# Performance work log

Hardware: AMD Instinct MI355X
Metric: run time of the kernel (lower is better)

Reference implementation:

```python
import jax, jax.numpy as jnp
import numpy as np

GAMMA = 0.9  # decay (init kwarg)


def setup_inputs() -> dict:
    key = jax.random.key(0)
    k0, k1, k2, k3 = jax.random.split(key, 4)
    B, T, D = 16, 2048, 256
    x = jax.random.normal(k0, (B, T, D), jnp.float32)
    scale = 1.0 / np.sqrt(D)
    Wq = jax.random.normal(k1, (D, D), jnp.float32) * scale
    Wk = jax.random.normal(k2, (D, D), jnp.float32) * scale
    Wv = jax.random.normal(k3, (D, D), jnp.float32) * scale
    return {"x": x, "Wq": Wq, "Wk": Wk, "Wv": Wv}


def reference(x, Wq, Wk, Wv):
    # x: [B, T, D]
    B, T, D = x.shape
    Q = x @ Wq  # [B, T, D]
    K = x @ Wk
    V = x @ Wv

    # Sequential retention recurrence over the [D, D] state:
    #   s[t] = gamma * s[t-1] + K[:, t, :]^T @ V[:, t, :]   (sums over batch, as in source)
    Kt = jnp.swapaxes(K, 0, 1)  # [T, B, D]
    Vt = jnp.swapaxes(V, 0, 1)  # [T, B, D]

    def step(s, kv):
        k_t, v_t = kv  # each [B, D]
        s = GAMMA * s + k_t.T @ v_t  # [D, D]
        return s, s.sum(-1)  # emit row-sum [D]

    # Loop runs t = 1 .. T-1 in the source (s starts at 0); s[0] := s[1].
    init = jnp.zeros((D, D), x.dtype)
    _, rows = jax.lax.scan(step, init, (Kt[1:], Vt[1:]))  # rows: [T-1, D]
    S = jnp.concatenate([rows[:1], rows], axis=0)  # [T, D]

    # Faithful to tf.reshape(S, [-1, seq_len]) then tf.transpose: a reshape-scramble,
    # NOT a plain transpose of S.
    S2 = S.reshape(D, T).T  # [T, D]
    return S2[None, :, :] * Q  # broadcast over batch -> [B, T, D]
```

## Files before the change

### kernel.cpp

```cpp
#include <hip/hip_runtime.h>
#include <hip/hip_bf16.h>
#include <math.h>


#define GAMMA_F 0.9f
#define T_LEN 2048
#define D_DIM 256
#define B_DIM 16
#define NCHUNK 32
#define CHUNK 64

typedef __attribute__((ext_vector_type(8))) short bf16x8;
typedef __attribute__((ext_vector_type(16))) float f32x16;

__device__ inline ushort f2bf(float f) {
    union { float f; unsigned u; } v; v.f = f;
    unsigned r = (v.u + 0x7FFFu + ((v.u >> 16) & 1u)) >> 16;
    return (ushort)r;
}

__global__ __launch_bounds__(256) void k_prep(const float* __restrict__ Wq,
                                              const float* __restrict__ Wk,
                                              const float* __restrict__ Wv,
                                              ushort* __restrict__ WqT,
                                              ushort* __restrict__ WkT,
                                              float* __restrict__ wv_sum) {
    int bid = blockIdx.x;
    int tid = threadIdx.x;
    if (bid < 32) {
        __shared__ float tile[64][68];
        const float* W = (bid < 16) ? Wq : Wk;
        ushort* WT = (bid < 16) ? WqT : WkT;
        int b = bid & 15;
        int k0 = (b & 3) * 64;
        int n0 = (b >> 2) * 64;
        int r = tid >> 4;
        int c4 = (tid & 15) * 4;
#pragma unroll
        for (int i = 0; i < 4; ++i) {
            float4 v = *(const float4*)(W + (size_t)(k0 + r + 16 * i) * D_DIM + n0 + c4);
            *(float4*)&tile[r + 16 * i][c4] = v;
        }
        __syncthreads();
        int n = tid >> 2;
        int j0 = (tid & 3) * 16;
        ushort tmp[16];
#pragma unroll
        for (int i = 0; i < 16; ++i) tmp[i] = f2bf(tile[j0 + i][n]);
        ushort* dst = WT + (size_t)(n0 + n) * D_DIM + k0 + j0;
#pragma unroll
        for (int i = 0; i < 16; ++i) dst[i] = tmp[i];
    } else {
        int j = (bid - 32) * 64 + (tid >> 2);
        int q = tid & 3;
        const float4* row4 = (const float4*)(Wv + (size_t)j * D_DIM + q * 64);
        float s = 0.f;
#pragma unroll
        for (int i = 0; i < 16; ++i) {
            float4 v = row4[i];
            s += v.x + v.y + v.z + v.w;
        }
        s += __shfl_xor(s, 1, 64);
        s += __shfl_xor(s, 2, 64);
        if (q == 0) wv_sum[j] = s;
    }
}

__global__ __launch_bounds__(256) void k_y(const float* __restrict__ x,
                                           const float* __restrict__ wv_sum,
                                           ushort* __restrict__ ybf,
                                           ushort* __restrict__ xbf) {
    int t = blockIdx.x;
    int d = threadIdx.x;
    float wvd = wv_sum[d];
    float xr[B_DIM];
#pragma unroll
    for (int b = 0; b < B_DIM; ++b)
        xr[b] = x[((size_t)b * T_LEN + t) * D_DIM + d];
#pragma unroll
    for (int b = 0; b < B_DIM; ++b)
        xbf[((size_t)b * T_LEN + t) * D_DIM + d] = f2bf(xr[b]);

    __shared__ float red[B_DIM][4];
    int wave = d >> 6, lane = d & 63;
#pragma unroll
    for (int b = 0; b < B_DIM; ++b) {
        float p = xr[b] * wvd;
        for (int o = 32; o > 0; o >>= 1) p += __shfl_down(p, o, 64);
        if (lane == 0) red[b][wave] = p;
    }
    __syncthreads();
    float yv = 0.f;
#pragma unroll
    for (int b = 0; b < B_DIM; ++b) {
        float wb = red[b][0] + red[b][1] + red[b][2] + red[b][3];
        yv += wb * xr[b];
    }
    ybf[(size_t)t * D_DIM + d] = f2bf(yv);
}

__global__ __launch_bounds__(256) void k_gmm(const ushort* __restrict__ ybf,
                                             const ushort* __restrict__ WkT,
                                             float* __restrict__ g) {
    __shared__ ushort As[32 * 64 * 8];
    __shared__ ushort Bs[32 * 64 * 8];
    int mt = blockIdx.x >> 2;
    int nt = blockIdx.x & 3;
    int tid = threadIdx.x, lane = tid & 63, w = tid >> 6;
    int wr = w >> 1, wc = w & 1, l31 = lane & 31, lh = lane >> 5;

#pragma unroll
    for (int i = 0; i < 8; ++i) {
        int slot = tid + 256 * i;
        int r = slot >> 5;
        int s2h = slot & 31;
        int rs = r ^ (s2h & 7);
        *(bf16x8*)&As[(s2h * 64 + rs) * 8] =
            *(const bf16x8*)&ybf[(size_t)(mt * 64 + r) * D_DIM + s2h * 8];
        *(bf16x8*)&Bs[(s2h * 64 + rs) * 8] =
            *(const bf16x8*)&WkT[(size_t)(nt * 64 + r) * D_DIM + s2h * 8];
    }
    __syncthreads();

    f32x16 acc;
#pragma unroll
    for (int e = 0; e < 16; ++e) acc[e] = 0.f;
#pragma unroll
    for (int s = 0; s < 16; ++s) {
        int s2h = s * 2 + lh;
        int ra = (wr * 32 + l31) ^ (s2h & 7);
        int rb = (wc * 32 + l31) ^ (s2h & 7);
        bf16x8 a = *(bf16x8*)&As[(s2h * 64 + ra) * 8];
        bf16x8 b = *(bf16x8*)&Bs[(s2h * 64 + rb) * 8];
        acc = __builtin_amdgcn_mfma_f32_32x32x16_bf16(a, b, acc, 0, 0, 0);
    }
#pragma unroll
    for (int reg = 0; reg < 16; ++reg) {
        int rr = (reg & 3) + 8 * (reg >> 2) + 4 * lh;
        g[(size_t)(mt * 64 + wr * 32 + rr) * D_DIM + nt * 64 + wc * 32 + l31] = acc[reg];
    }
}

__global__ void k_scanA(const float* __restrict__ g, float* __restrict__ loc,
                        float* __restrict__ carry) {
    int c = blockIdx.x;
    int d = threadIdx.x;
    float acc = 0.f;
    int base = c * CHUNK;
#pragma unroll
    for (int o8 = 0; o8 < 8; ++o8) {
        float v[8];
#pragma unroll
        for (int j = 0; j < 8; ++j) {
            int t = base + o8 * 8 + j;
            v[j] = (t == 0) ? 0.f : g[(size_t)t * D_DIM + d];
        }
#pragma unroll
        for (int j = 0; j < 8; ++j) {
            acc = GAMMA_F * acc + v[j];
            loc[(size_t)(base + o8 * 8 + j) * D_DIM + d] = acc;
        }
    }
    carry[(size_t)c * D_DIM + d] = acc;
}

__global__ __launch_bounds__(256) void k_S2P(const float* __restrict__ loc,
                                             const float* __restrict__ carry,
                                             float* __restrict__ S2) {
    int tp = blockIdx.x;
    int r = threadIdx.x;
    int src = (tp == 0) ? 1 : tp;
    int c = src >> 6, o = src & 63;
    const float g64 = 1.1790184577738601e-03f;
    float p = 0.f;
    for (int j = 0; j < c; ++j)
        p = p * g64 + carry[(size_t)j * D_DIM + r];
    const float log2g = -0.15200309344504995f;
    float gp = exp2f((float)(o + 1) * log2g);
    float Aval = loc[(size_t)src * D_DIM + r] + gp * p;
    int trow = ((tp & 7) << 8) + r;
    int dcol = tp >> 3;
    S2[(size_t)trow * D_DIM + dcol] = Aval;
}

__global__ __launch_bounds__(256) void k_qgemm(const ushort* __restrict__ xbf,
                                               const ushort* __restrict__ WqT,
                                               const float* __restrict__ S2,
                                               float* __restrict__ out) {
    __shared__ ushort As[8 * 128 * 8];
    __shared__ ushort Bs[8 * 128 * 8];
    int bid = blockIdx.x;
    int mb = bid >> 1;
    int nb = bid & 1;
    int tid = threadIdx.x;
    int lane = tid & 63, w = tid >> 6;
    int wr = w >> 1, wc = w & 1;
    int l31 = lane & 31, lh = lane >> 5;

    f32x16 acc[2][2];
#pragma unroll
    for (int i = 0; i < 2; ++i)
#pragma unroll
        for (int j = 0; j < 2; ++j)
#pragma unroll
            for (int e = 0; e < 16; ++e) acc[i][j][e] = 0.f;

    int r = tid >> 1;
    int h0 = tid & 1;
    const ushort* ag = xbf + (size_t)(mb * 128 + r) * D_DIM + h0 * 32;
    const ushort* bg = WqT + (size_t)(nb * 128 + r) * D_DIM + h0 * 32;

    for (int kb = 0; kb < 4; ++kb) {
#pragma unroll
        for (int j = 0; j < 4; ++j) {
            bf16x8 av = *(const bf16x8*)(ag + kb * 64 + j * 8);
            *(bf16x8*)&As[((h0 * 4 + j) * 128 + r) * 8] = av;
            bf16x8 bv = *(const bf16x8*)(bg + kb * 64 + j * 8);
            *(bf16x8*)&Bs[((h0 * 4 + j) * 128 + r) * 8] = bv;
        }
        __syncthreads();
#pragma unroll
        for (int s = 0; s < 4; ++s) {
            int c0 = (s * 2 + lh) * 128;
            bf16x8 a0 = *(bf16x8*)&As[(c0 + wr * 64 + l31) * 8];
            bf16x8 a1 = *(bf16x8*)&As[(c0 + wr * 64 + 32 + l31) * 8];
            bf16x8 b0 = *(bf16x8*)&Bs[(c0 + wc * 64 + l31) * 8];
            bf16x8 b1 = *(bf16x8*)&Bs[(c0 + wc * 64 + 32 + l31) * 8];
            acc[0][0] = __builtin_amdgcn_mfma_f32_32x32x16_bf16(a0, b0, acc[0][0], 0, 0, 0);
            acc[0][1] = __builtin_amdgcn_mfma_f32_32x32x16_bf16(a0, b1, acc[0][1], 0, 0, 0);
            acc[1][0] = __builtin_amdgcn_mfma_f32_32x32x16_bf16(a1, b0, acc[1][0], 0, 0, 0);
            acc[1][1] = __builtin_amdgcn_mfma_f32_32x32x16_bf16(a1, b1, acc[1][1], 0, 0, 0);
        }
        __syncthreads();
    }

    int t_base = (mb & 15) * 128;
    size_t row_base = (size_t)mb * 128;
#pragma unroll
    for (int mi = 0; mi < 2; ++mi) {
#pragma unroll
        for (int ni = 0; ni < 2; ++ni) {
            int gn = nb * 128 + wc * 64 + ni * 32 + l31;
#pragma unroll
            for (int reg = 0; reg < 16; ++reg) {
                int rr = (reg & 3) + 8 * (reg >> 2) + 4 * lh;
                int m = wr * 64 + mi * 32 + rr;
                float s2v = S2[(size_t)(t_base + m) * D_DIM + gn];
                out[(row_base + m) * D_DIM + gn] = acc[mi][ni][reg] * s2v;
            }
        }
    }
}

extern "C" void kernel_launch(void* const* d_in, const int* in_sizes, int n_in,
                              void* d_out, int out_size, void* d_ws, size_t ws_size,
                              hipStream_t stream) {
    const float* x  = (const float*)d_in[0];
    const float* Wq = (const float*)d_in[1];
    const float* Wk = (const float*)d_in[2];
    const float* Wv = (const float*)d_in[3];
    float* out = (float*)d_out;

    float* ws = (float*)d_ws;
    float* g      = ws;
    float* loc    = g + 524288;
    float* S2     = loc + 524288;
    float* wv_sum = S2 + 524288;
    float* carry  = wv_sum + 256;
    ushort* WqT   = (ushort*)(carry + 8192);
    ushort* WkT   = WqT + 65536;
    ushort* ybf   = WkT + 65536;
    ushort* xbf   = ybf + 524288;

    k_prep<<<36, 256, 0, stream>>>(Wq, Wk, Wv, WqT, WkT, wv_sum);
    k_y<<<T_LEN, 256, 0, stream>>>(x, wv_sum, ybf, xbf);
    k_gmm<<<128, 256, 0, stream>>>(ybf, WkT, g);
    k_scanA<<<NCHUNK, 256, 0, stream>>>(g, loc, carry);
    k_S2P<<<T_LEN, 256, 0, stream>>>(loc, carry, S2);
    k_qgemm<<<(B_DIM * T_LEN / 128) * 2, 256, 0, stream>>>(xbf, WqT, S2, out);
}
```

Before: 128.9 us.

## Fuse all stages into one cooperative persistent kernel with grid syncs

Replaces the six-kernel launch chain with a single cooperative kernel of 256 blocks × 1024 threads that runs the prep, y-projection, K GEMM, chunked scan, prefix fix-up and Q GEMM stages, separated by grid.sync(). The scan chunk size drops to 8 and the prefix carry loop is truncated to the last 32 chunks, since gamma^256 is negligible. The GEMMs now load MFMA operands straight from global memory instead of staging them through LDS. The previous multi-kernel path is kept as a fallback if the cooperative launch fails. This removes launch gaps and the long serial carry loop, at the risk of low occupancy from 1024-thread blocks and uncoalesced operand loads.

```diff
diff --git a/kernel.cpp b/kernel.cpp
--- a/kernel.cpp
+++ b/kernel.cpp
@@ -1,14 +1,15 @@
 #include <hip/hip_runtime.h>
 #include <hip/hip_bf16.h>
+#include <hip/hip_cooperative_groups.h>
 #include <math.h>
+
+namespace cg = cooperative_groups;
 
 
 #define GAMMA_F 0.9f
 #define T_LEN 2048
 #define D_DIM 256
 #define B_DIM 16
-#define NCHUNK 32
-#define CHUNK 64
 
 typedef __attribute__((ext_vector_type(8))) short bf16x8;
 typedef __attribute__((ext_vector_type(16))) float f32x16;
@@ -17,6 +18,168 @@
     union { float f; unsigned u; } v; v.f = f;
     unsigned r = (v.u + 0x7FFFu + ((v.u >> 16) & 1u)) >> 16;
     return (ushort)r;
+}
+
+__global__ __launch_bounds__(1024) void k_mega(
+        const float* __restrict__ x, const float* __restrict__ Wq,
+        const float* __restrict__ Wk, const float* __restrict__ Wv,
+        float* __restrict__ out,
+        ushort* __restrict__ WqT, ushort* __restrict__ WkT,
+        float* __restrict__ wv_sum, ushort* __restrict__ ybf,
+        ushort* __restrict__ xbf, float* __restrict__ g,
+        float* __restrict__ loc, float* __restrict__ carry,
+        float* __restrict__ S2) {
+    cg::grid_group grid = cg::this_grid();
+    int bid = blockIdx.x, tid = threadIdx.x;
+    __shared__ float red[4][B_DIM][4];
+
+    if (bid == 0 && tid < 256) {
+        const float4* row4 = (const float4*)(Wv + (size_t)tid * D_DIM);
+        float s = 0.f;
+#pragma unroll
+        for (int i = 0; i < 64; ++i) {
+            float4 v = row4[i];
+            s += v.x + v.y + v.z + v.w;
+        }
+        wv_sum[tid] = s;
+    } else if (bid >= 1 && bid < 9) {
+        int half = (bid - 1) >> 2;
+        const float* W = half ? Wk : Wq;
+        ushort* WT = half ? WkT : WqT;
+        int gth = ((bid - 1) & 3) * 1024 + tid;
+        int n = gth >> 4, k0 = (gth & 15) * 16;
+        ushort tmp[16];
+#pragma unroll
+        for (int i = 0; i < 16; ++i) tmp[i] = f2bf(W[(size_t)(k0 + i) * D_DIM + n]);
+#pragma unroll
+        for (int i = 0; i < 4; ++i)
+            *(ushort4*)&WT[(size_t)n * D_DIM + k0 + i * 4] = *(ushort4*)&tmp[i * 4];
+    }
+    grid.sync();
+
+    {
+        int sub = tid >> 8, d = tid & 255, lane = tid & 63, wv = (tid >> 6) & 3;
+        float wvd = wv_sum[d];
+#pragma unroll
+        for (int it = 0; it < 2; ++it) {
+            int t = it * 1024 + bid * 4 + sub;
+            float xr[B_DIM];
+#pragma unroll
+            for (int b = 0; b < B_DIM; ++b)
+                xr[b] = x[((size_t)b * T_LEN + t) * D_DIM + d];
+#pragma unroll
+            for (int b = 0; b < B_DIM; ++b)
+                xbf[((size_t)b * T_LEN + t) * D_DIM + d] = f2bf(xr[b]);
+#pragma unroll
+            for (int b = 0; b < B_DIM; ++b) {
+                float p = xr[b] * wvd;
+                for (int o = 32; o > 0; o >>= 1) p += __shfl_down(p, o, 64);
+                if (lane == 0) red[sub][b][wv] = p;
+            }
+            __syncthreads();
+            float yv = 0.f;
+#pragma unroll
+            for (int b = 0; b < B_DIM; ++b) {
+                float wb = red[sub][b][0] + red[sub][b][1] + red[sub][b][2] + red[sub][b][3];
+                yv += wb * xr[b];
+            }
+            ybf[(size_t)t * D_DIM + d] = f2bf(yv);
+            __syncthreads();
+        }
+    }
+    grid.sync();
+
+    if (bid < 128 && tid < 256) {
+        int w = tid >> 6, lane = tid & 63;
+        int mt = bid >> 2, nt = bid & 3;
+        int wr = w >> 1, wc = w & 1, l31 = lane & 31, lh = lane >> 5;
+        f32x16 acc;
+#pragma unroll
+        for (int e = 0; e < 16; ++e) acc[e] = 0.f;
+        const ushort* abase = ybf + (size_t)(mt * 64 + wr * 32 + l31) * D_DIM + lh * 8;
+        const ushort* bbase = WkT + (size_t)(nt * 64 + wc * 32 + l31) * D_DIM + lh * 8;
+#pragma unroll
+        for (int s = 0; s < 16; ++s) {
+            bf16x8 a = *(const bf16x8*)(abase + s * 16);
+            bf16x8 b = *(const bf16x8*)(bbase + s * 16);
+            acc = __builtin_amdgcn_mfma_f32_32x32x16_bf16(a, b, acc, 0, 0, 0);
+        }
+#pragma unroll
+        for (int reg = 0; reg < 16; ++reg) {
+            int rr = (reg & 3) + 8 * (reg >> 2) + 4 * lh;
+            g[(size_t)(mt * 64 + wr * 32 + rr) * D_DIM + nt * 64 + wc * 32 + l31] = acc[reg];
+        }
+    }
+    grid.sync();
+
+    if (tid < 256) {
+        int c = bid, d = tid;
+        float v[8];
+#pragma unroll
+        for (int j = 0; j < 8; ++j) {
+            int t = c * 8 + j;
+            v[j] = (t == 0) ? 0.f : g[(size_t)t * D_DIM + d];
+        }
+        float acc = 0.f;
+#pragma unroll
+        for (int j = 0; j < 8; ++j) {
+            acc = GAMMA_F * acc + v[j];
+            loc[(size_t)(c * 8 + j) * D_DIM + d] = acc;
+        }
+        carry[(size_t)c * D_DIM + d] = acc;
+    }
+    grid.sync();
+
+    {
+        int sub = tid >> 8, r = tid & 255;
+        const float g8 = 0.43046721f;
+        const float log2g = -0.15200309344504995f;
+#pragma unroll
+        for (int it = 0; it < 2; ++it) {
+            int tp = it * 1024 + bid * 4 + sub;
+            int src = (tp == 0) ? 1 : tp;
+            int c = src >> 3, o = src & 7;
+            int j0 = c - 32; if (j0 < 0) j0 = 0;
+            float p = 0.f;
+            for (int j = j0; j < c; ++j)
+                p = p * g8 + carry[(size_t)j * D_DIM + r];
+            float gp = exp2f((float)(o + 1) * log2g);
+            float Aval = loc[(size_t)src * D_DIM + r] + gp * p;
+            S2[(size_t)(((tp & 7) << 8) + r) * D_DIM + (tp >> 3)] = Aval;
+        }
+    }
+    grid.sync();
+
+    {
+        int w = tid >> 6, lane = tid & 63;
+        int wr = w >> 2, wc = w & 3, l31 = lane & 31, lh = lane >> 5;
+        int mb = bid;
+        int t_base = (mb & 15) * 128;
+        const ushort* abase = xbf + (size_t)(mb * 128 + wr * 32 + l31) * D_DIM + lh * 8;
+        bf16x8 afr[16];
+#pragma unroll
+        for (int s = 0; s < 16; ++s) afr[s] = *(const bf16x8*)(abase + s * 16);
+#pragma unroll
+        for (int nb = 0; nb < 2; ++nb) {
+            const ushort* bbase = WqT + (size_t)(nb * 128 + wc * 32 + l31) * D_DIM + lh * 8;
+            f32x16 acc;
+#pragma unroll
+            for (int e = 0; e < 16; ++e) acc[e] = 0.f;
+#pragma unroll
+            for (int s = 0; s < 16; ++s) {
+                bf16x8 b = *(const bf16x8*)(bbase + s * 16);
+                acc = __builtin_amdgcn_mfma_f32_32x32x16_bf16(afr[s], b, acc, 0, 0, 0);
+            }
+            int gn = nb * 128 + wc * 32 + l31;
+#pragma unroll
+            for (int reg = 0; reg < 16; ++reg) {
+                int rr = (reg & 3) + 8 * (reg >> 2) + 4 * lh;
+                int m = wr * 32 + rr;
+                float s2v = S2[(size_t)(t_base + m) * D_DIM + gn];
+                out[((size_t)mb * 128 + m) * D_DIM + gn] = acc[reg] * s2v;
+            }
+        }
+    }
 }
 
 __global__ __launch_bounds__(256) void k_prep(const float* __restrict__ Wq,
@@ -102,36 +265,19 @@
 __global__ __launch_bounds__(256) void k_gmm(const ushort* __restrict__ ybf,
                                              const ushort* __restrict__ WkT,
                                              float* __restrict__ g) {
-    __shared__ ushort As[32 * 64 * 8];
-    __shared__ ushort Bs[32 * 64 * 8];
     int mt = blockIdx.x >> 2;
     int nt = blockIdx.x & 3;
     int tid = threadIdx.x, lane = tid & 63, w = tid >> 6;
     int wr = w >> 1, wc = w & 1, l31 = lane & 31, lh = lane >> 5;
-
-#pragma unroll
-    for (int i = 0; i < 8; ++i) {
-        int slot = tid + 256 * i;
-        int r = slot >> 5;
-        int s2h = slot & 31;
-        int rs = r ^ (s2h & 7);
-        *(bf16x8*)&As[(s2h * 64 + rs) * 8] =
-            *(const bf16x8*)&ybf[(size_t)(mt * 64 + r) * D_DIM + s2h * 8];
-        *(bf16x8*)&Bs[(s2h * 64 + rs) * 8] =
-            *(const bf16x8*)&WkT[(size_t)(nt * 64 + r) * D_DIM + s2h * 8];
-    }
-    __syncthreads();
-
     f32x16 acc;
 #pragma unroll
     for (int e = 0; e < 16; ++e) acc[e] = 0.f;
+    const ushort* abase = ybf + (size_t)(mt * 64 + wr * 32 + l31) * D_DIM + lh * 8;
+    const ushort* bbase = WkT + (size_t)(nt * 64 + wc * 32 + l31) * D_DIM + lh * 8;
 #pragma unroll
     for (int s = 0; s < 16; ++s) {
-        int s2h = s * 2 + lh;
-        int ra = (wr * 32 + l31) ^ (s2h & 7);
-        int rb = (wc * 32 + l31) ^ (s2h & 7);
-        bf16x8 a = *(bf16x8*)&As[(s2h * 64 + ra) * 8];
-        bf16x8 b = *(bf16x8*)&Bs[(s2h * 64 + rb) * 8];
+        bf16x8 a = *(const bf16x8*)(abase + s * 16);
+        bf16x8 b = *(const bf16x8*)(bbase + s * 16);
         acc = __builtin_amdgcn_mfma_f32_32x32x16_bf16(a, b, acc, 0, 0, 0);
     }
 #pragma unroll
@@ -145,21 +291,17 @@
                         float* __restrict__ carry) {
     int c = blockIdx.x;
     int d = threadIdx.x;
+    float v[8];
+#pragma unroll
+    for (int j = 0; j < 8; ++j) {
+        int t = c * 8 + j;
+        v[j] = (t == 0) ? 0.f : g[(size_t)t * D_DIM + d];
+    }
     float acc = 0.f;
-    int base = c * CHUNK;
-#pragma unroll
-    for (int o8 = 0; o8 < 8; ++o8) {
-        float v[8];
-#pragma unroll
-        for (int j = 0; j < 8; ++j) {
-            int t = base + o8 * 8 + j;
-            v[j] = (t == 0) ? 0.f : g[(size_t)t * D_DIM + d];
-        }
-#pragma unroll
-        for (int j = 0; j < 8; ++j) {
-            acc = GAMMA_F * acc + v[j];
-            loc[(size_t)(base + o8 * 8 + j) * D_DIM + d] = acc;
-        }
+#pragma unroll
+    for (int j = 0; j < 8; ++j) {
+        acc = GAMMA_F * acc + v[j];
+        loc[(size_t)(c * 8 + j) * D_DIM + d] = acc;
     }
     carry[(size_t)c * D_DIM + d] = acc;
 }
@@ -170,11 +312,12 @@
     int tp = blockIdx.x;
     int r = threadIdx.x;
     int src = (tp == 0) ? 1 : tp;
-    int c = src >> 6, o = src & 63;
-    const float g64 = 1.1790184577738601e-03f;
+    int c = src >> 3, o = src & 7;
+    const float g8 = 0.43046721f;
+    int j0 = c - 32; if (j0 < 0) j0 = 0;
     float p = 0.f;
-    for (int j = 0; j < c; ++j)
-        p = p * g64 + carry[(size_t)j * D_DIM + r];
+    for (int j = j0; j < c; ++j)
+        p = p * g8 + carry[(size_t)j * D_DIM + r];
     const float log2g = -0.15200309344504995f;
     float gp = exp2f((float)(o + 1) * log2g);
     float Aval = loc[(size_t)src * D_DIM + r] + gp * p;
@@ -187,16 +330,12 @@
                                                const ushort* __restrict__ WqT,
                                                const float* __restrict__ S2,
                                                float* __restrict__ out) {
-    __shared__ ushort As[8 * 128 * 8];
-    __shared__ ushort Bs[8 * 128 * 8];
     int bid = blockIdx.x;
     int mb = bid >> 1;
     int nb = bid & 1;
     int tid = threadIdx.x;
     int lane = tid & 63, w = tid >> 6;
-    int wr = w >> 1, wc = w & 1;
-    int l31 = lane & 31, lh = lane >> 5;
-
+    int wr = w >> 1, wc = w & 1, l31 = lane & 31, lh = lane >> 5;
     f32x16 acc[2][2];
 #pragma unroll
     for (int i = 0; i < 2; ++i)
@@ -204,36 +343,19 @@
         for (int j = 0; j < 2; ++j)
 #pragma unroll
             for (int e = 0; e < 16; ++e) acc[i][j][e] = 0.f;
-
-    int r = tid >> 1;
-    int h0 = tid & 1;
-    const ushort* ag = xbf + (size_t)(mb * 128 + r) * D_DIM + h0 * 32;
-    const ushort* bg = WqT + (size_t)(nb * 128 + r) * D_DIM + h0 * 32;
-
-    for (int kb = 0; kb < 4; ++kb) {
-#pragma unroll
-        for (int j = 0; j < 4; ++j) {
-            bf16x8 av = *(const bf16x8*)(ag + kb * 64 + j * 8);
-            *(bf16x8*)&As[((h0 * 4 + j) * 128 + r) * 8] = av;
-            bf16x8 bv = *(const bf16x8*)(bg + kb * 64 + j * 8);
-            *(bf16x8*)&Bs[((h0 * 4 + j) * 128 + r) * 8] = bv;
-        }
-        __syncthreads();
-#pragma unroll
-        for (int s = 0; s < 4; ++s) {
-            int c0 = (s * 2 + lh) * 128;
-            bf16x8 a0 = *(bf16x8*)&As[(c0 + wr * 64 + l31) * 8];
-            bf16x8 a1 = *(bf16x8*)&As[(c0 + wr * 64 + 32 + l31) * 8];
-            bf16x8 b0 = *(bf16x8*)&Bs[(c0 + wc * 64 + l31) * 8];
-            bf16x8 b1 = *(bf16x8*)&Bs[(c0 + wc * 64 + 32 + l31) * 8];
-            acc[0][0] = __builtin_amdgcn_mfma_f32_32x32x16_bf16(a0, b0, acc[0][0], 0, 0, 0);
-            acc[0][1] = __builtin_amdgcn_mfma_f32_32x32x16_bf16(a0, b1, acc[0][1], 0, 0, 0);
-            acc[1][0] = __builtin_amdgcn_mfma_f32_32x32x16_bf16(a1, b0, acc[1][0], 0, 0, 0);
-            acc[1][1] = __builtin_amdgcn_mfma_f32_32x32x16_bf16(a1, b1, acc[1][1], 0, 0, 0);
-        }
-        __syncthreads();
-    }
-
+#pragma unroll
+    for (int s = 0; s < 16; ++s) {
+        const ushort* ab = xbf + (size_t)(mb * 128 + wr * 64 + l31) * D_DIM + s * 16 + lh * 8;
+        const ushort* bb = WqT + (size_t)(nb * 128 + wc * 64 + l31) * D_DIM + s * 16 + lh * 8;
+        bf16x8 a0 = *(const bf16x8*)ab;
+        bf16x8 a1 = *(const bf16x8*)(ab + 32 * D_DIM);
+        bf16x8 b0 = *(const bf16x8*)bb;
+        bf16x8 b1 = *(const bf16x8*)(bb + 32 * D_DIM);
+        acc[0][0] = __builtin_amdgcn_mfma_f32_32x32x16_bf16(a0, b0, acc[0][0], 0, 0, 0);
+        acc[0][1] = __builtin_amdgcn_mfma_f32_32x32x16_bf16(a0, b1, acc[0][1], 0, 0, 0);
+        acc[1][0] = __builtin_amdgcn_mfma_f32_32x32x16_bf16(a1, b0, acc[1][0], 0, 0, 0);
+        acc[1][1] = __builtin_amdgcn_mfma_f32_32x32x16_bf16(a1, b1, acc[1][1], 0, 0, 0);
+    }
     int t_base = (mb & 15) * 128;
     size_t row_base = (size_t)mb * 128;
 #pragma unroll
@@ -267,15 +389,22 @@
     float* S2     = loc + 524288;
     float* wv_sum = S2 + 524288;
     float* carry  = wv_sum + 256;
-    ushort* WqT   = (ushort*)(carry + 8192);
+    ushort* WqT   = (ushort*)(carry + 65536);
     ushort* WkT   = WqT + 65536;
     ushort* ybf   = WkT + 65536;
     ushort* xbf   = ybf + 524288;
 
-    k_prep<<<36, 256, 0, stream>>>(Wq, Wk, Wv, WqT, WkT, wv_sum);
-    k_y<<<T_LEN, 256, 0, stream>>>(x, wv_sum, ybf, xbf);
-    k_gmm<<<128, 256, 0, stream>>>(ybf, WkT, g);
-    k_scanA<<<NCHUNK, 256, 0, stream>>>(g, loc, carry);
-    k_S2P<<<T_LEN, 256, 0, stream>>>(loc, carry, S2);
-    k_qgemm<<<(B_DIM * T_LEN / 128) * 2, 256, 0, stream>>>(xbf, WqT, S2, out);
-}
+    void* args[] = {(void*)&x, (void*)&Wq, (void*)&Wk, (void*)&Wv, (void*)&out,
+                    (void*)&WqT, (void*)&WkT, (void*)&wv_sum, (void*)&ybf,
+                    (void*)&xbf, (void*)&g, (void*)&loc, (void*)&carry, (void*)&S2};
+    hipError_t e = hipLaunchCooperativeKernel((void*)k_mega, dim3(256), dim3(1024),
+                                              args, 0, stream);
+    if (e != hipSuccess) {
+        k_prep<<<36, 256, 0, stream>>>(Wq, Wk, Wv, WqT, WkT, wv_sum);
+        k_y<<<T_LEN, 256, 0, stream>>>(x, wv_sum, ybf, xbf);
+        k_gmm<<<128, 256, 0, stream>>>(ybf, WkT, g);
+        k_scanA<<<256, 256, 0, stream>>>(g, loc, carry);
+        k_S2P<<<T_LEN, 256, 0, stream>>>(loc, carry, S2);
+        k_qgemm<<<(B_DIM * T_LEN / 128) * 2, 256, 0, stream>>>(xbf, WqT, S2, out);
+    }
+}
```

Result: slower. 300.4 us (+133.2%).

## Shrink scan chunks to 8 with truncated carry sum; stage full-K tiles in qgemm

Applied to the files above, without the earlier changes.

The chunked scan now uses 256 chunks of 8 steps instead of 32 chunks of 64, which spreads the sequential work over more blocks. The prefix carry in k_S2P is truncated to the last 32 chunks, relying on gamma^256 being negligible. The Q GEMM kernel now loads the full K=256 A tile into LDS once and loops over both N halves in one block, which halves the A reloads but raises LDS use to 64KB per block and lowers block count and occupancy. The carry workspace offset is enlarged to fit the larger carry array.

```diff
diff --git a/kernel.cpp b/kernel.cpp
--- a/kernel.cpp
+++ b/kernel.cpp
@@ -7,8 +7,6 @@
 #define T_LEN 2048
 #define D_DIM 256
 #define B_DIM 16
-#define NCHUNK 32
-#define CHUNK 64
 
 typedef __attribute__((ext_vector_type(8))) short bf16x8;
 typedef __attribute__((ext_vector_type(16))) float f32x16;
@@ -145,21 +143,17 @@
                         float* __restrict__ carry) {
     int c = blockIdx.x;
     int d = threadIdx.x;
+    float v[8];
+#pragma unroll
+    for (int j = 0; j < 8; ++j) {
+        int t = c * 8 + j;
+        v[j] = (t == 0) ? 0.f : g[(size_t)t * D_DIM + d];
+    }
     float acc = 0.f;
-    int base = c * CHUNK;
-#pragma unroll
-    for (int o8 = 0; o8 < 8; ++o8) {
-        float v[8];
-#pragma unroll
-        for (int j = 0; j < 8; ++j) {
-            int t = base + o8 * 8 + j;
-            v[j] = (t == 0) ? 0.f : g[(size_t)t * D_DIM + d];
-        }
-#pragma unroll
-        for (int j = 0; j < 8; ++j) {
-            acc = GAMMA_F * acc + v[j];
-            loc[(size_t)(base + o8 * 8 + j) * D_DIM + d] = acc;
-        }
+#pragma unroll
+    for (int j = 0; j < 8; ++j) {
+        acc = GAMMA_F * acc + v[j];
+        loc[(size_t)(c * 8 + j) * D_DIM + d] = acc;
     }
     carry[(size_t)c * D_DIM + d] = acc;
 }
@@ -170,11 +164,12 @@
     int tp = blockIdx.x;
     int r = threadIdx.x;
     int src = (tp == 0) ? 1 : tp;
-    int c = src >> 6, o = src & 63;
-    const float g64 = 1.1790184577738601e-03f;
+    int c = src >> 3, o = src & 7;
+    const float g8 = 0.43046721f;
+    int j0 = c - 32; if (j0 < 0) j0 = 0;
     float p = 0.f;
-    for (int j = 0; j < c; ++j)
-        p = p * g64 + carry[(size_t)j * D_DIM + r];
+    for (int j = j0; j < c; ++j)
+        p = p * g8 + carry[(size_t)j * D_DIM + r];
     const float log2g = -0.15200309344504995f;
     float gp = exp2f((float)(o + 1) * log2g);
     float Aval = loc[(size_t)src * D_DIM + r] + gp * p;
@@ -187,40 +182,46 @@
                                                const ushort* __restrict__ WqT,
                                                const float* __restrict__ S2,
                                                float* __restrict__ out) {
-    __shared__ ushort As[8 * 128 * 8];
-    __shared__ ushort Bs[8 * 128 * 8];
-    int bid = blockIdx.x;
-    int mb = bid >> 1;
-    int nb = bid & 1;
+    __shared__ ushort As[32 * 128 * 8];
+    __shared__ ushort Bs[32 * 128 * 8];
+    int mb = blockIdx.x;
     int tid = threadIdx.x;
     int lane = tid & 63, w = tid >> 6;
-    int wr = w >> 1, wc = w & 1;
-    int l31 = lane & 31, lh = lane >> 5;
-
-    f32x16 acc[2][2];
-#pragma unroll
-    for (int i = 0; i < 2; ++i)
-#pragma unroll
-        for (int j = 0; j < 2; ++j)
-#pragma unroll
-            for (int e = 0; e < 16; ++e) acc[i][j][e] = 0.f;
-
-    int r = tid >> 1;
-    int h0 = tid & 1;
+    int wr = w >> 1, wc = w & 1, l31 = lane & 31, lh = lane >> 5;
+    int r = tid >> 1, h0 = tid & 1;
+
     const ushort* ag = xbf + (size_t)(mb * 128 + r) * D_DIM + h0 * 32;
-    const ushort* bg = WqT + (size_t)(nb * 128 + r) * D_DIM + h0 * 32;
-
-    for (int kb = 0; kb < 4; ++kb) {
-#pragma unroll
-        for (int j = 0; j < 4; ++j) {
-            bf16x8 av = *(const bf16x8*)(ag + kb * 64 + j * 8);
-            *(bf16x8*)&As[((h0 * 4 + j) * 128 + r) * 8] = av;
-            bf16x8 bv = *(const bf16x8*)(bg + kb * 64 + j * 8);
-            *(bf16x8*)&Bs[((h0 * 4 + j) * 128 + r) * 8] = bv;
-        }
+#pragma unroll
+    for (int kb = 0; kb < 4; ++kb)
+#pragma unroll
+        for (int j = 0; j < 4; ++j)
+            *(bf16x8*)&As[((kb * 8 + h0 * 4 + j) * 128 + r) * 8] =
+                *(const bf16x8*)(ag + kb * 64 + j * 8);
+
+    int t_base = (mb & 15) * 128;
+    size_t row_base = (size_t)mb * 128;
+
+    for (int nb = 0; nb < 2; ++nb) {
+        if (nb) __syncthreads();
+        const ushort* bg = WqT + (size_t)(nb * 128 + r) * D_DIM + h0 * 32;
+#pragma unroll
+        for (int kb = 0; kb < 4; ++kb)
+#pragma unroll
+            for (int j = 0; j < 4; ++j)
+                *(bf16x8*)&Bs[((kb * 8 + h0 * 4 + j) * 128 + r) * 8] =
+                    *(const bf16x8*)(bg + kb * 64 + j * 8);
         __syncthreads();
-#pragma unroll
-        for (int s = 0; s < 4; ++s) {
+
+        f32x16 acc[2][2];
+#pragma unroll
+        for (int i = 0; i < 2; ++i)
+#pragma unroll
+            for (int j = 0; j < 2; ++j)
+#pragma unroll
+                for (int e = 0; e < 16; ++e) acc[i][j][e] = 0.f;
+
+#pragma unroll
+        for (int s = 0; s < 16; ++s) {
             int c0 = (s * 2 + lh) * 128;
             bf16x8 a0 = *(bf16x8*)&As[(c0 + wr * 64 + l31) * 8];
             bf16x8 a1 = *(bf16x8*)&As[(c0 + wr * 64 + 32 + l31) * 8];
@@ -231,22 +232,19 @@
             acc[1][0] = __builtin_amdgcn_mfma_f32_32x32x16_bf16(a1, b0, acc[1][0], 0, 0, 0);
             acc[1][1] = __builtin_amdgcn_mfma_f32_32x32x16_bf16(a1, b1, acc[1][1], 0, 0, 0);
         }
-        __syncthreads();
-    }
-
-    int t_base = (mb & 15) * 128;
-    size_t row_base = (size_t)mb * 128;
-#pragma unroll
-    for (int mi = 0; mi < 2; ++mi) {
-#pragma unroll
-        for (int ni = 0; ni < 2; ++ni) {
-            int gn = nb * 128 + wc * 64 + ni * 32 + l31;
-#pragma unroll
-            for (int reg = 0; reg < 16; ++reg) {
-                int rr = (reg & 3) + 8 * (reg >> 2) + 4 * lh;
-                int m = wr * 64 + mi * 32 + rr;
-                float s2v = S2[(size_t)(t_base + m) * D_DIM + gn];
-                out[(row_base + m) * D_DIM + gn] = acc[mi][ni][reg] * s2v;
+
+#pragma unroll
+        for (int mi = 0; mi < 2; ++mi) {
+#pragma unroll
+            for (int ni = 0; ni < 2; ++ni) {
+                int gn = nb * 128 + wc * 64 + ni * 32 + l31;
+#pragma unroll
+                for (int reg = 0; reg < 16; ++reg) {
+                    int rr = (reg & 3) + 8 * (reg >> 2) + 4 * lh;
+                    int m = wr * 64 + mi * 32 + rr;
+                    float s2v = S2[(size_t)(t_base + m) * D_DIM + gn];
+                    out[(row_base + m) * D_DIM + gn] = acc[mi][ni][reg] * s2v;
+                }
             }
         }
     }
@@ -267,7 +265,7 @@
     float* S2     = loc + 524288;
     float* wv_sum = S2 + 524288;
     float* carry  = wv_sum + 256;
-    ushort* WqT   = (ushort*)(carry + 8192);
+    ushort* WqT   = (ushort*)(carry + 65536);
     ushort* WkT   = WqT + 65536;
     ushort* ybf   = WkT + 65536;
     ushort* xbf   = ybf + 524288;
@@ -275,7 +273,7 @@
     k_prep<<<36, 256, 0, stream>>>(Wq, Wk, Wv, WqT, WkT, wv_sum);
     k_y<<<T_LEN, 256, 0, stream>>>(x, wv_sum, ybf, xbf);
     k_gmm<<<128, 256, 0, stream>>>(ybf, WkT, g);
-    k_scanA<<<NCHUNK, 256, 0, stream>>>(g, loc, carry);
+    k_scanA<<<256, 256, 0, stream>>>(g, loc, carry);
     k_S2P<<<T_LEN, 256, 0, stream>>>(loc, carry, S2);
-    k_qgemm<<<(B_DIM * T_LEN / 128) * 2, 256, 0, stream>>>(xbf, WqT, S2, out);
-}
+    k_qgemm<<<256, 256, 0, stream>>>(xbf, WqT, S2, out);
+}
```

Result: no change. 130.8 us (+1.5%).

## Fuse K-projection GEMM with chunked scan and restructure carry propagation

Applied to the files above, without the earlier changes.

Merges the g GEMM and the local scan into one kernel. Each block computes a 64x256 tile of g with MFMA, reading WkT straight from global memory, stages the result in LDS, and runs 8-step sub-chunk scans directly. This removes the g round trip through global memory and one launch. Carries now sit at a granularity of 8 steps, so k_S2P keeps a running prefix across 64 consecutive columns. It truncates the history to 32 carries, relying on gamma decay, and writes S2 as coalesced float4 rows through an LDS transpose. The cost is far fewer blocks (32 instead of 2048 or 128), so parallelism drops sharply and each thread runs a long serial loop.

```diff
diff --git a/kernel.cpp b/kernel.cpp
--- a/kernel.cpp
+++ b/kernel.cpp
@@ -7,8 +7,6 @@
 #define T_LEN 2048
 #define D_DIM 256
 #define B_DIM 16
-#define NCHUNK 32
-#define CHUNK 64
 
 typedef __attribute__((ext_vector_type(8))) short bf16x8;
 typedef __attribute__((ext_vector_type(16))) float f32x16;
@@ -99,15 +97,16 @@
     ybf[(size_t)t * D_DIM + d] = f2bf(yv);
 }
 
-__global__ __launch_bounds__(256) void k_gmm(const ushort* __restrict__ ybf,
-                                             const ushort* __restrict__ WkT,
-                                             float* __restrict__ g) {
-    __shared__ ushort As[32 * 64 * 8];
-    __shared__ ushort Bs[32 * 64 * 8];
-    int mt = blockIdx.x >> 2;
-    int nt = blockIdx.x & 3;
+__global__ __launch_bounds__(256) void k_gs(const ushort* __restrict__ ybf,
+                                            const ushort* __restrict__ WkT,
+                                            float* __restrict__ loc,
+                                            float* __restrict__ carry) {
+    __shared__ char smem[65536];
+    ushort* As = (ushort*)smem;
+    float* Cs = (float*)smem;
+    int mt = blockIdx.x;
     int tid = threadIdx.x, lane = tid & 63, w = tid >> 6;
-    int wr = w >> 1, wc = w & 1, l31 = lane & 31, lh = lane >> 5;
+    int l31 = lane & 31, lh = lane >> 5;
 
 #pragma unroll
     for (int i = 0; i < 8; ++i) {
@@ -117,70 +116,97 @@
         int rs = r ^ (s2h & 7);
         *(bf16x8*)&As[(s2h * 64 + rs) * 8] =
             *(const bf16x8*)&ybf[(size_t)(mt * 64 + r) * D_DIM + s2h * 8];
-        *(bf16x8*)&Bs[(s2h * 64 + rs) * 8] =
-            *(const bf16x8*)&WkT[(size_t)(nt * 64 + r) * D_DIM + s2h * 8];
-    }
-    __syncthreads();
-
-    f32x16 acc;
-#pragma unroll
-    for (int e = 0; e < 16; ++e) acc[e] = 0.f;
+    }
+    __syncthreads();
+
+    f32x16 acc[2][2];
+#pragma unroll
+    for (int i = 0; i < 2; ++i)
+#pragma unroll
+        for (int j = 0; j < 2; ++j)
+#pragma unroll
+            for (int e = 0; e < 16; ++e) acc[i][j][e] = 0.f;
+
+    const ushort* bq = WkT + (size_t)(w * 64 + l31) * D_DIM + lh * 8;
 #pragma unroll
     for (int s = 0; s < 16; ++s) {
         int s2h = s * 2 + lh;
-        int ra = (wr * 32 + l31) ^ (s2h & 7);
-        int rb = (wc * 32 + l31) ^ (s2h & 7);
-        bf16x8 a = *(bf16x8*)&As[(s2h * 64 + ra) * 8];
-        bf16x8 b = *(bf16x8*)&Bs[(s2h * 64 + rb) * 8];
-        acc = __builtin_amdgcn_mfma_f32_32x32x16_bf16(a, b, acc, 0, 0, 0);
-    }
-#pragma unroll
-    for (int reg = 0; reg < 16; ++reg) {
-        int rr = (reg & 3) + 8 * (reg >> 2) + 4 * lh;
-        g[(size_t)(mt * 64 + wr * 32 + rr) * D_DIM + nt * 64 + wc * 32 + l31] = acc[reg];
-    }
-}
-
-__global__ void k_scanA(const float* __restrict__ g, float* __restrict__ loc,
-                        float* __restrict__ carry) {
-    int c = blockIdx.x;
-    int d = threadIdx.x;
-    float acc = 0.f;
-    int base = c * CHUNK;
-#pragma unroll
-    for (int o8 = 0; o8 < 8; ++o8) {
-        float v[8];
+        bf16x8 a0 = *(bf16x8*)&As[(s2h * 64 + (l31 ^ (s2h & 7))) * 8];
+        bf16x8 a1 = *(bf16x8*)&As[(s2h * 64 + ((32 + l31) ^ (s2h & 7))) * 8];
+        bf16x8 b0 = *(const bf16x8*)(bq + s * 16);
+        bf16x8 b1 = *(const bf16x8*)(bq + 32 * D_DIM + s * 16);
+        acc[0][0] = __builtin_amdgcn_mfma_f32_32x32x16_bf16(a0, b0, acc[0][0], 0, 0, 0);
+        acc[0][1] = __builtin_amdgcn_mfma_f32_32x32x16_bf16(a0, b1, acc[0][1], 0, 0, 0);
+        acc[1][0] = __builtin_amdgcn_mfma_f32_32x32x16_bf16(a1, b0, acc[1][0], 0, 0, 0);
+        acc[1][1] = __builtin_amdgcn_mfma_f32_32x32x16_bf16(a1, b1, acc[1][1], 0, 0, 0);
+    }
+    __syncthreads();
+
+#pragma unroll
+    for (int mi = 0; mi < 2; ++mi)
+#pragma unroll
+        for (int ni = 0; ni < 2; ++ni) {
+            int n = w * 64 + ni * 32 + l31;
+#pragma unroll
+            for (int reg = 0; reg < 16; ++reg) {
+                int rr = (reg & 3) + 8 * (reg >> 2) + 4 * lh;
+                Cs[(mi * 32 + rr) * D_DIM + n] = acc[mi][ni][reg];
+            }
+        }
+    __syncthreads();
+
+    int d = tid;
+#pragma unroll
+    for (int cl = 0; cl < 8; ++cl) {
+        float a = 0.f;
 #pragma unroll
         for (int j = 0; j < 8; ++j) {
-            int t = base + o8 * 8 + j;
-            v[j] = (t == 0) ? 0.f : g[(size_t)t * D_DIM + d];
-        }
-#pragma unroll
-        for (int j = 0; j < 8; ++j) {
-            acc = GAMMA_F * acc + v[j];
-            loc[(size_t)(base + o8 * 8 + j) * D_DIM + d] = acc;
-        }
-    }
-    carry[(size_t)c * D_DIM + d] = acc;
+            int tl = cl * 8 + j;
+            int gt = mt * 64 + tl;
+            float v = (gt == 0) ? 0.f : Cs[tl * D_DIM + d];
+            a = GAMMA_F * a + v;
+            loc[(size_t)gt * D_DIM + d] = a;
+        }
+        carry[(size_t)(mt * 8 + cl) * D_DIM + d] = a;
+    }
 }
 
 __global__ __launch_bounds__(256) void k_S2P(const float* __restrict__ loc,
                                              const float* __restrict__ carry,
                                              float* __restrict__ S2) {
-    int tp = blockIdx.x;
+    __shared__ float buf[64 * 256];
+    int q = blockIdx.x & 7;
+    int dc0 = (blockIdx.x >> 3) * 64;
     int r = threadIdx.x;
-    int src = (tp == 0) ? 1 : tp;
-    int c = src >> 6, o = src & 63;
-    const float g64 = 1.1790184577738601e-03f;
-    float p = 0.f;
-    for (int j = 0; j < c; ++j)
-        p = p * g64 + carry[(size_t)j * D_DIM + r];
+    const float g8 = 0.43046721f;
     const float log2g = -0.15200309344504995f;
-    float gp = exp2f((float)(o + 1) * log2g);
-    float Aval = loc[(size_t)src * D_DIM + r] + gp * p;
-    int trow = ((tp & 7) << 8) + r;
-    int dcol = tp >> 3;
-    S2[(size_t)trow * D_DIM + dcol] = Aval;
+    float gp = exp2f((float)(q + 1) * log2g);
+
+    float P = 0.f;
+    int j0 = dc0 - 32; if (j0 < 0) j0 = 0;
+    for (int j = j0; j < dc0; ++j)
+        P = P * g8 + carry[(size_t)j * D_DIM + r];
+
+    for (int i = 0; i < 64; ++i) {
+        int dcol = dc0 + i;
+        int tp = dcol * 8 + q;
+        int src = (tp == 0) ? 1 : tp;
+        float Aval = loc[(size_t)src * D_DIM + r] + gp * P;
+        buf[i * 256 + r] = Aval;
+        P = P * g8 + carry[(size_t)dcol * D_DIM + r];
+    }
+    __syncthreads();
+
+    float* dst = S2 + (size_t)(q * 256 + r) * D_DIM + dc0;
+#pragma unroll
+    for (int i4 = 0; i4 < 16; ++i4) {
+        float4 v;
+        v.x = buf[(i4 * 4 + 0) * 256 + r];
+        v.y = buf[(i4 * 4 + 1) * 256 + r];
+        v.z = buf[(i4 * 4 + 2) * 256 + r];
+        v.w = buf[(i4 * 4 + 3) * 256 + r];
+        *(float4*)(dst + i4 * 4) = v;
+    }
 }
 
 __global__ __launch_bounds__(256) void k_qgemm(const ushort* __restrict__ xbf,
@@ -262,20 +288,18 @@
     float* out = (float*)d_out;
 
     float* ws = (float*)d_ws;
-    float* g      = ws;
-    float* loc    = g + 524288;
+    float* loc    = ws;
     float* S2     = loc + 524288;
     float* wv_sum = S2 + 524288;
     float* carry  = wv_sum + 256;
-    ushort* WqT   = (ushort*)(carry + 8192);
+    ushort* WqT   = (ushort*)(carry + 65536);
     ushort* WkT   = WqT + 65536;
     ushort* ybf   = WkT + 65536;
     ushort* xbf   = ybf + 524288;
 
     k_prep<<<36, 256, 0, stream>>>(Wq, Wk, Wv, WqT, WkT, wv_sum);
     k_y<<<T_LEN, 256, 0, stream>>>(x, wv_sum, ybf, xbf);
-    k_gmm<<<128, 256, 0, stream>>>(ybf, WkT, g);
-    k_scanA<<<NCHUNK, 256, 0, stream>>>(g, loc, carry);
-    k_S2P<<<T_LEN, 256, 0, stream>>>(loc, carry, S2);
+    k_gs<<<32, 256, 0, stream>>>(ybf, WkT, loc, carry);
+    k_S2P<<<32, 256, 0, stream>>>(loc, carry, S2);
     k_qgemm<<<(B_DIM * T_LEN / 128) * 2, 256, 0, stream>>>(xbf, WqT, S2, out);
 }
```

New measurement: 135.2 us. 4.9% more time.
